# Kernel tuning notes

Hardware: AMD Instinct MI355X
Metric: run time of the kernel (lower is better)

Reference implementation:

```python
import jax, jax.numpy as jnp
import numpy as np

B_, L, DM = 2, 1024, 1024
DIN = 2048            # expand * d_model
HD = 64               # headdim
NH = DIN // HD        # 32 heads
DS = 64               # d_state
NG = 1                # ngroups
TH = NH * (DS // 2)   # theta dim = 1024
SPLITS = np.cumsum([DIN, DIN, NG * DS, NG * DS, NH, TH]).tolist()
EPS = 1e-5

def _rms(x, w):
    return x * jax.lax.rsqrt(jnp.mean(x * x, -1, keepdims=True) + EPS) * w

def setup_inputs():
    ks = jax.random.split(jax.random.key(0), 8)
    d_in = 2 * DIN + 2 * NG * DS + NH + TH + NH  # 5312
    u = jax.random.normal(ks[0], (B_, L, DM), jnp.float32)
    in_proj_w = jax.random.normal(ks[1], (d_in, DM), jnp.float32) * 0.02
    out_proj_w = jax.random.normal(ks[2], (DM, DIN), jnp.float32) * 0.02
    # dt_bias init as in module: inv-softplus of dt ~ logUniform(dt_min, dt_max)
    dt = jnp.exp(jax.random.uniform(ks[3], (NH,)) * (np.log(0.1) - np.log(0.001)) + np.log(0.001))
    dt_bias = dt + jnp.log(-jnp.expm1(-dt))
    A_log = jnp.log(jax.random.uniform(ks[4], (NH,), minval=1.0, maxval=16.0))
    D = jnp.ones((NH,), jnp.float32)
    B_norm_w = jnp.ones((DS,), jnp.float32)
    C_norm_w = jnp.ones((DS,), jnp.float32)
    B_bias = jnp.ones((NH, DS), jnp.float32)
    C_bias = jnp.ones((NH, DS), jnp.float32)
    norm_w = jnp.ones((DIN,), jnp.float32)
    return dict(u=u, in_proj_w=in_proj_w, dt_bias=dt_bias, A_log=A_log, D=D,
                B_norm_w=B_norm_w, C_norm_w=C_norm_w, B_bias=B_bias, C_bias=C_bias,
                norm_w=norm_w, out_proj_w=out_proj_w)

def reference(u, in_proj_w, dt_bias, A_log, D, B_norm_w, C_norm_w, B_bias, C_bias, norm_w, out_proj_w):
    zxbcdt = u @ in_proj_w.T                                  # (b,l,5312)
    z, x, Br, Cr, dtr, thr, lamr = jnp.split(zxbcdt, SPLITS, axis=-1)
    dt = jax.nn.softplus(dtr + dt_bias)                       # (b,l,h)
    A = -jnp.exp(A_log)                                       # (h,) negative
    x = x.reshape(B_, L, NH, HD)
    # BC norm at group level, then group->head expansion, then head-specific bias
    Bg = _rms(Br.reshape(B_, L, NG, DS), B_norm_w)
    Cg = _rms(Cr.reshape(B_, L, NG, DS), C_norm_w)
    Bh = jnp.broadcast_to(Bg, (B_, L, NH, DS)) + B_bias
    Ch = jnp.broadcast_to(Cg, (B_, L, NH, DS)) + C_bias
    # data-dependent RoPE with cumulative angles
    th_cs = jnp.cumsum(thr.reshape(B_, L, NH, DS // 2), axis=1)
    c, s = jnp.cos(th_cs), jnp.sin(th_cs)
    def rot(v):
        v1, v2 = v[..., :DS // 2], v[..., DS // 2:]
        return jnp.concatenate([v1 * c - v2 * s, v1 * s + v2 * c], -1)
    Bh, Ch = rot(Bh), rot(Ch)
    # trapezoidal discretization coefficients
    lam = jax.nn.sigmoid(lamr)                                # (b,l,h) in [0,1]
    alpha = jnp.exp(dt * A)
    gamma = lam * dt
    beta = (1.0 - lam) * dt * alpha
    def step(carry, inp):
        h, bx_prev = carry
        x_t, B_t, C_t, a_t, b_t, g_t = inp
        bx = x_t[..., :, None] * B_t[..., None, :]            # (b,h,p,n)
        h = a_t[..., None, None] * h + b_t[..., None, None] * bx_prev + g_t[..., None, None] * bx
        y = jnp.einsum('bhn,bhpn->bhp', C_t, h)
        return (h, bx), y
    m = lambda t: jnp.moveaxis(t, 1, 0)                       # seq-major for scan
    h0 = jnp.zeros((B_, NH, HD, DS), u.dtype)
    _, ys = jax.lax.scan(step, (h0, h0), (m(x), m(Bh), m(Ch), m(alpha), m(beta), m(gamma)))
    y = jnp.moveaxis(ys, 0, 1) + x * D[:, None]               # D skip, per head
    y = y.reshape(B_, L, DIN)
    # RMSNormGated, norm_before_gate=False: norm(y * silu(z)) * w
    g = y * jax.nn.silu(z)
    out = _rms(g, norm_w)
    return out @ out_proj_w.T
```

## Files before the change

### kernel.cpp

```cpp
#include <hip/hip_runtime.h>
#include <hip/hip_bf16.h>

#define DMODEL 1024
#define DIN    2048
#define NH     32
#define HD     64
#define DS     64
#define LSEQ   1024
#define BB     2
#define DTOT   5312
#define ROWS   (BB*LSEQ)
#define OFF_Z   0
#define OFF_X   2048
#define OFF_BR  4096
#define OFF_CR  4160
#define OFF_DT  4224
#define OFF_TH  4256
#define OFF_LAM 5280
#define NZX     4096
#define NREM    (DTOT - NZX)
#define NSEG 8
#define SEG  (LSEQ / NSEG)

typedef short  s16x8 __attribute__((ext_vector_type(8)));
typedef float  f32x4 __attribute__((ext_vector_type(4)));
typedef unsigned short u16;

__device__ __forceinline__ unsigned int f2bf(float f) {
    unsigned int u = __float_as_uint(f);
    u += 0x7fffu + ((u >> 16) & 1u);
    return u >> 16;
}
__device__ __forceinline__ unsigned int pk(float x, float y) {
    return f2bf(x) | (f2bf(y) << 16);
}
__device__ __forceinline__ void split1(float v, u16& hi, u16& lo) {
    const unsigned int h = f2bf(v);
    hi = (u16)h;
    lo = (u16)f2bf(v - __uint_as_float(h << 16));
}

typedef const __attribute__((address_space(1))) unsigned int glb_u32;
typedef __attribute__((address_space(3))) unsigned int lds_u32;
__device__ __forceinline__ void gload16(const void* g, void* l) {
    __builtin_amdgcn_global_load_lds((glb_u32*)g, (lds_u32*)l, 16, 0, 0);
}

__global__ __launch_bounds__(256) void conv_u(const float* __restrict__ src,
        u16* __restrict__ hi, u16* __restrict__ lo) {
    const size_t i4 = ((size_t)blockIdx.x * 256 + threadIdx.x) * 4;
    const float4 v = *(const float4*)(src + i4);
    const unsigned int h0 = f2bf(v.x), h1 = f2bf(v.y), h2 = f2bf(v.z), h3 = f2bf(v.w);
    uint2 hw, lw;
    hw.x = h0 | (h1 << 16); hw.y = h2 | (h3 << 16);
    lw.x = pk(v.x - __uint_as_float(h0 << 16), v.y - __uint_as_float(h1 << 16));
    lw.y = pk(v.z - __uint_as_float(h2 << 16), v.w - __uint_as_float(h3 << 16));
    *(uint2*)(hi + i4) = hw;
    *(uint2*)(lo + i4) = lw;
}

__global__ __launch_bounds__(256) void conv_w(const float* __restrict__ src,
        u16* __restrict__ hi, u16* __restrict__ lo) {
    const size_t i4 = ((size_t)blockIdx.x * 256 + threadIdx.x) * 4;
    const float4 v = *(const float4*)(src + i4);
    const unsigned int h0 = f2bf(v.x), h1 = f2bf(v.y), h2 = f2bf(v.z), h3 = f2bf(v.w);
    uint2 hw, lw;
    hw.x = h0 | (h1 << 16); hw.y = h2 | (h3 << 16);
    lw.x = pk(v.x - __uint_as_float(h0 << 16), v.y - __uint_as_float(h1 << 16));
    lw.y = pk(v.z - __uint_as_float(h2 << 16), v.w - __uint_as_float(h3 << 16));
    *(uint2*)(hi + i4) = hw;
    if ((i4 >> 10) >= NZX)
        *(uint2*)(lo + (i4 - (size_t)NZX * DMODEL)) = lw;
}

__global__ __launch_bounds__(256) void conv_wo(const float* __restrict__ src,
        u16* __restrict__ hi) {
    const size_t i4 = ((size_t)blockIdx.x * 256 + threadIdx.x) * 4;
    const float4 v = *(const float4*)(src + i4);
    uint2 hw;
    hw.x = pk(v.x, v.y); hw.y = pk(v.z, v.w);
    *(uint2*)(hi + i4) = hw;
}

__global__ __launch_bounds__(256) void mfma_gemm_zx(const u16* __restrict__ uA_,
                                                    const u16* __restrict__ uW,
                                                    float* __restrict__ zx) {
    __shared__ u16 Al[2][128 * 32];
    __shared__ u16 Bl[2][128 * 32];
    const int tid = threadIdx.x;
    const int m0 = blockIdx.y * 128, n0 = blockIdx.x * 128;
    const int lane = tid & 63, wave = tid >> 6;
    const int wr = wave >> 1, wc = wave & 1;
    const int lr = lane >> 4, lc = lane & 15;
    const int sr = tid >> 2;
    const int sc = (tid & 3) * 8;

    f32x4 acc[4][4] = {};

    const u16* pA = uA_ + (size_t)(m0 + sr) * DMODEL + sc;
    const u16* pB = uW  + (size_t)(n0 + sr) * DMODEL + sc;

#define STAGE_ZX(buf, k0) {                                              \
        gload16(pA + (k0), &Al[buf][tid * 8]);                           \
        gload16(pA + (k0) + (size_t)64 * DMODEL, &Al[buf][tid * 8 + 2048]); \
        gload16(pB + (k0), &Bl[buf][tid * 8]);                           \
        gload16(pB + (k0) + (size_t)64 * DMODEL, &Bl[buf][tid * 8 + 2048]); }

    STAGE_ZX(0, 0);
    __syncthreads();
    int cur = 0;
    for (int k0 = 0; k0 < DMODEL; k0 += 32) {
        if (k0 + 32 < DMODEL) STAGE_ZX(cur ^ 1, k0 + 32);
        s16x8 af[4], bf[4];
        #pragma unroll
        for (int f = 0; f < 4; ++f) {
            af[f] = *(const s16x8*)&Al[cur][(wr * 64 + f * 16 + lc) * 32 + lr * 8];
            bf[f] = *(const s16x8*)&Bl[cur][(wc * 64 + f * 16 + lc) * 32 + lr * 8];
        }
        #pragma unroll
        for (int fm = 0; fm < 4; ++fm)
            #pragma unroll
            for (int fn = 0; fn < 4; ++fn)
                acc[fm][fn] = __builtin_amdgcn_mfma_f32_16x16x32_bf16(
                    af[fm], bf[fn], acc[fm][fn], 0, 0, 0);
        __syncthreads();
        cur ^= 1;
    }
#undef STAGE_ZX

    #pragma unroll
    for (int fm = 0; fm < 4; ++fm)
        #pragma unroll
        for (int fn = 0; fn < 4; ++fn) {
            const size_t col = n0 + wc * 64 + fn * 16 + lc;
            #pragma unroll
            for (int j = 0; j < 4; ++j) {
                const size_t row = m0 + wr * 64 + fm * 16 + lr * 4 + j;
                zx[row * DTOT + col] = acc[fm][fn][j];
            }
        }
}

__global__ __launch_bounds__(256) void mfma_gemm_out(const u16* __restrict__ A,
                                                     const u16* __restrict__ B,
                                                     float* __restrict__ C,
                                                     int K, int ldc) {
    __shared__ u16 Als[2][128 * 32];
    __shared__ u16 Bls[2][64 * 32];
    const int tid = threadIdx.x;
    const int m0 = blockIdx.y * 128, n0 = blockIdx.x * 64;
    const int lane = tid & 63, wave = tid >> 6;
    const int wr = wave >> 1, wc = wave & 1;
    const int lr = lane >> 4, lc = lane & 15;
    const int sr = tid >> 2;
    const int sc = (tid & 3) * 8;

    f32x4 acc[4][2] = {};

    const u16* pA = A + (size_t)(m0 + sr) * K + sc;
    const u16* pB = B + (size_t)(n0 + sr) * K + sc;

#define STAGE_OUT(buf, k0) {                                             \
        gload16(pA + (k0), &Als[buf][tid * 8]);                          \
        gload16(pA + (k0) + (size_t)64 * K, &Als[buf][tid * 8 + 2048]);  \
        gload16(pB + (k0), &Bls[buf][tid * 8]); }

    STAGE_OUT(0, 0);
    __syncthreads();
    int cur = 0;
    for (int k0 = 0; k0 < K; k0 += 32) {
        if (k0 + 32 < K) STAGE_OUT(cur ^ 1, k0 + 32);
        s16x8 af[4], bf[2];
        #pragma unroll
        for (int f = 0; f < 4; ++f)
            af[f] = *(const s16x8*)&Als[cur][(wr * 64 + f * 16 + lc) * 32 + lr * 8];
        #pragma unroll
        for (int f = 0; f < 2; ++f)
            bf[f] = *(const s16x8*)&Bls[cur][(wc * 32 + f * 16 + lc) * 32 + lr * 8];
        #pragma unroll
        for (int fm = 0; fm < 4; ++fm)
            #pragma unroll
            for (int fn = 0; fn < 2; ++fn)
                acc[fm][fn] = __builtin_amdgcn_mfma_f32_16x16x32_bf16(
                    af[fm], bf[fn], acc[fm][fn], 0, 0, 0);
        __syncthreads();
        cur ^= 1;
    }
#undef STAGE_OUT

    #pragma unroll
    for (int fm = 0; fm < 4; ++fm)
        #pragma unroll
        for (int fn = 0; fn < 2; ++fn) {
            const size_t col = n0 + wc * 32 + fn * 16 + lc;
            #pragma unroll
            for (int j = 0; j < 4; ++j) {
                const size_t row = m0 + wr * 64 + fm * 16 + lr * 4 + j;
                C[row * (size_t)ldc + col] = acc[fm][fn][j];
            }
        }
}

__global__ __launch_bounds__(256) void mfma_gemm_rem3(const u16* __restrict__ uh,
        const u16* __restrict__ ul, const u16* __restrict__ wh,
        const u16* __restrict__ wl, float* __restrict__ zxr) {
    __shared__ u16 Ah[2][128 * 32], Alo[2][128 * 32];
    __shared__ u16 Bh[2][64 * 32],  Blo[2][64 * 32];
    const int tid = threadIdx.x;
    const int m0 = blockIdx.y * 128, n0 = blockIdx.x * 64;
    const int lane = tid & 63, wave = tid >> 6;
    const int wr = wave >> 1, wc = wave & 1;
    const int lr = lane >> 4, lc = lane & 15;
    const int sr = tid >> 2;
    const int sc = (tid & 3) * 8;

    f32x4 acc[4][2] = {};

    const u16* pAh = uh + (size_t)(m0 + sr) * DMODEL + sc;
    const u16* pAl = ul + (size_t)(m0 + sr) * DMODEL + sc;
    const u16* pBh = wh + (size_t)(n0 + sr) * DMODEL + sc;
    const u16* pBl = wl + (size_t)(n0 + sr) * DMODEL + sc;

#define STAGE_R3(buf, k0) {                                                  \
        gload16(pAh + (k0), &Ah[buf][tid * 8]);                              \
        gload16(pAh + (k0) + (size_t)64 * DMODEL, &Ah[buf][tid * 8 + 2048]); \
        gload16(pAl + (k0), &Alo[buf][tid * 8]);                             \
        gload16(pAl + (k0) + (size_t)64 * DMODEL, &Alo[buf][tid * 8 + 2048]);\
        gload16(pBh + (k0), &Bh[buf][tid * 8]);                              \
        gload16(pBl + (k0), &Blo[buf][tid * 8]); }

    STAGE_R3(0, 0);
    __syncthreads();
    int cur = 0;
    for (int k0 = 0; k0 < DMODEL; k0 += 32) {
        if (k0 + 32 < DMODEL) STAGE_R3(cur ^ 1, k0 + 32);
        s16x8 ahf[4], alf[4], bhf[2], blf[2];
        #pragma unroll
        for (int f = 0; f < 4; ++f) {
            ahf[f] = *(const s16x8*)&Ah[cur][(wr * 64 + f * 16 + lc) * 32 + lr * 8];
            alf[f] = *(const s16x8*)&Alo[cur][(wr * 64 + f * 16 + lc) * 32 + lr * 8];
        }
        #pragma unroll
        for (int f = 0; f < 2; ++f) {
            bhf[f] = *(const s16x8*)&Bh[cur][(wc * 32 + f * 16 + lc) * 32 + lr * 8];
            blf[f] = *(const s16x8*)&Blo[cur][(wc * 32 + f * 16 + lc) * 32 + lr * 8];
        }
        #pragma unroll
        for (int fm = 0; fm < 4; ++fm)
            #pragma unroll
            for (int fn = 0; fn < 2; ++fn) {
                acc[fm][fn] = __builtin_amdgcn_mfma_f32_16x16x32_bf16(
                    ahf[fm], bhf[fn], acc[fm][fn], 0, 0, 0);
                acc[fm][fn] = __builtin_amdgcn_mfma_f32_16x16x32_bf16(
                    ahf[fm], blf[fn], acc[fm][fn], 0, 0, 0);
                acc[fm][fn] = __builtin_amdgcn_mfma_f32_16x16x32_bf16(
                    alf[fm], bhf[fn], acc[fm][fn], 0, 0, 0);
            }
        __syncthreads();
        cur ^= 1;
    }
#undef STAGE_R3

    #pragma unroll
    for (int fm = 0; fm < 4; ++fm)
        #pragma unroll
        for (int fn = 0; fn < 2; ++fn) {
            const size_t col = n0 + wc * 32 + fn * 16 + lc;
            #pragma unroll
            for (int j = 0; j < 4; ++j) {
                const size_t row = m0 + wr * 64 + fm * 16 + lr * 4 + j;
                zxr[row * DTOT + col] = acc[fm][fn][j];
            }
        }
}

__global__ __launch_bounds__(64) void prep_kernel(const float* __restrict__ zx,
        const float* __restrict__ dt_bias, const float* __restrict__ A_log,
        const float* __restrict__ B_norm_w, const float* __restrict__ C_norm_w,
        float* __restrict__ Bg, float* __restrict__ Cg,
        float4* __restrict__ abg4) {
    const int bl = blockIdx.x;
    const int b = bl >> 10, l = bl & (LSEQ - 1);
    const int t  = threadIdx.x;
    const float* row = zx + (size_t)bl * DTOT;
    const float br = row[OFF_BR + t];
    const float cr = row[OFF_CR + t];
    float ssb = br * br, ssc = cr * cr;
    #pragma unroll
    for (int k = 1; k < 64; k <<= 1) { ssb += __shfl_xor(ssb, k); ssc += __shfl_xor(ssc, k); }
    const float scB = rsqrtf(ssb * (1.f / 64.f) + 1e-5f);
    const float scC = rsqrtf(ssc * (1.f / 64.f) + 1e-5f);
    Bg[(size_t)bl * 64 + t] = br * scB * B_norm_w[t];
    Cg[(size_t)bl * 64 + t] = cr * scC * C_norm_w[t];
    if (t < NH) {
        const float dtr = row[OFF_DT + t] + dt_bias[t];
        const float dt  = (dtr > 20.f) ? dtr : log1pf(expf(dtr));
        const float lamr = row[OFF_LAM + t];
        const float lam  = 1.f / (1.f + expf(-lamr));
        const float Ah   = -expf(A_log[t]);
        const float al   = expf(dt * Ah);
        const float bp   = (1.f - lam) * dt;
        const size_t o = ((size_t)b * NH + t) * LSEQ + l;
        abg4[o] = make_float4(al, bp * al, lam * dt, bp);
    }
}

__global__ __launch_bounds__(256) void cumsum_kernel(const float* __restrict__ zx,
                                                     float* __restrict__ th_cs) {
    const int bh = blockIdx.x;
    const int b = bh >> 5, h = bh & 31;
    const int d = threadIdx.x & 31, seg = threadIdx.x >> 5;
    const float* base = zx + (size_t)b * LSEQ * DTOT + OFF_TH + h * 32 + d;
    float* out = th_cs + (size_t)b * LSEQ * 1024 + h * 32 + d;
    __shared__ float sums[8][33];
    const int l0 = seg * 128;
    float s = 0.f;
    #pragma unroll 4
    for (int i = 0; i < 128; ++i) s += base[(size_t)(l0 + i) * DTOT];
    sums[seg][d] = s;
    __syncthreads();
    float acc = 0.f;
    for (int s2 = 0; s2 < seg; ++s2) acc += sums[s2][d];
    #pragma unroll 4
    for (int i = 0; i < 128; ++i) {
        acc += base[(size_t)(l0 + i) * DTOT];
        out[(size_t)(l0 + i) * 1024] = acc;
    }
}

__global__ __launch_bounds__(256) void rot_kernel(const float* __restrict__ th_cs,
        const float* __restrict__ Bg, const float* __restrict__ Cg,
        const float* __restrict__ B_bias, const float* __restrict__ C_bias,
        float* __restrict__ Brot, float* __restrict__ Crot) {
    const size_t idx = (size_t)blockIdx.x * 256 + threadIdx.x;
    const int j = (int)(idx & 31);
    const int h = (int)((idx >> 5) & 31);
    const size_t bl = idx >> 10;
    const int l = (int)(bl & (LSEQ - 1));
    const int b = (int)(bl >> 10);
    const float th = th_cs[idx];
    float s, c;
    sincosf(th, &s, &c);
    float v1 = Bg[bl * 64 + j]      + B_bias[h * 64 + j];
    float v2 = Bg[bl * 64 + 32 + j] + B_bias[h * 64 + 32 + j];
    const size_t ob = ((size_t)(b * NH + h) * LSEQ + l) * DS + j;
    Brot[ob]      = v1 * c - v2 * s;
    Brot[ob + 32] = v1 * s + v2 * c;
    v1 = Cg[bl * 64 + j]      + C_bias[h * 64 + j];
    v2 = Cg[bl * 64 + 32 + j] + C_bias[h * 64 + 32 + j];
    Crot[ob]      = v1 * c - v2 * s;
    Crot[ob + 32] = v1 * s + v2 * c;
}

__global__ __launch_bounds__(64) void wcalc_kernel(const float4* __restrict__ abg4,
        float* __restrict__ wbuf, float* __restrict__ aprod,
        float* __restrict__ bscale, float* __restrict__ Lbuf) {
    const int bh = blockIdx.x;
    const int lane = threadIdx.x;
    const int seg = lane >> 3, sub = lane & 7;
    const int t0 = seg * SEG;
    const int sbase = t0 + sub * 16;
    const float4* ab = abg4 + (size_t)bh * LSEQ;

    float part = 0.f;
    #pragma unroll
    for (int i = 0; i < 16; ++i) part += logf(ab[sbase + i].x);
    float incl = part;
    #pragma unroll
    for (int d = 1; d < 8; d <<= 1) {
        const float v = __shfl_up(incl, d, 8);
        if (sub >= d) incl += v;
    }
    const float LE = __shfl(incl, 7, 8);
    float Lrun = incl - part;

    for (int i = 0; i < 16; ++i) {
        const int s = sbase + i;
        const float4 A = ab[s];
        Lrun += logf(A.x);
        Lbuf[(size_t)bh * LSEQ + s] = Lrun;
        float w;
        if ((s & (SEG - 1)) == (SEG - 1)) w = A.z;
        else w = __expf(LE - Lrun) * (A.z + ab[s + 1].w);
        wbuf[(size_t)bh * LSEQ + s] = w;
    }
    if (sub == 0) {
        aprod[bh * NSEG + seg] = __expf(LE);
        bscale[bh * NSEG + seg] = (seg > 0) ? __expf(LE) * ab[t0].w : 0.f;
    }
}

#define WK 136
__global__ __launch_bounds__(256) void hseg_gemm(const float* __restrict__ zx,
        const float* __restrict__ Brot, const float* __restrict__ wbuf,
        float* __restrict__ hseg) {
    __shared__ u16 XH[64][WK], XL[64][WK], BHs[64][WK], BLs[64][WK];
    const int blk = blockIdx.x;
    const int seg = blk & (NSEG - 1), bh = blk >> 3;
    const int b = bh >> 5, h = bh & 31;
    const int tid = threadIdx.x;

    {
        const int sIdx = tid >> 1, half = tid & 1;
        const int t = seg * SEG + sIdx;
        const float wv = wbuf[(size_t)bh * LSEQ + t];
        const float* xsrc = zx + ((size_t)b * LSEQ + t) * DTOT + OFF_X + h * 64 + half * 32;
        const float* bsrc = Brot + ((size_t)bh * LSEQ + t) * DS + half * 32;
        #pragma unroll
        for (int i = 0; i < 32; i += 4) {
            const float4 xv = *(const float4*)(xsrc + i);
            const float4 bv = *(const float4*)(bsrc + i);
            const int p0 = half * 32 + i;
            u16 hi, lo;
            split1(xv.x * wv, hi, lo); XH[p0 + 0][sIdx] = hi; XL[p0 + 0][sIdx] = lo;
            split1(xv.y * wv, hi, lo); XH[p0 + 1][sIdx] = hi; XL[p0 + 1][sIdx] = lo;
            split1(xv.z * wv, hi, lo); XH[p0 + 2][sIdx] = hi; XL[p0 + 2][sIdx] = lo;
            split1(xv.w * wv, hi, lo); XH[p0 + 3][sIdx] = hi; XL[p0 + 3][sIdx] = lo;
            split1(bv.x, hi, lo); BHs[p0 + 0][sIdx] = hi; BLs[p0 + 0][sIdx] = lo;
            split1(bv.y, hi, lo); BHs[p0 + 1][sIdx] = hi; BLs[p0 + 1][sIdx] = lo;
            split1(bv.z, hi, lo); BHs[p0 + 2][sIdx] = hi; BLs[p0 + 2][sIdx] = lo;
            split1(bv.w, hi, lo); BHs[p0 + 3][sIdx] = hi; BLs[p0 + 3][sIdx] = lo;
        }
    }
    __syncthreads();

    const int lane = tid & 63, wave = tid >> 6;
    const int wR = wave >> 1, wC = wave & 1;
    const int lr = lane >> 4, lc = lane & 15;

    f32x4 acc[2][2] = {};
    #pragma unroll
    for (int ks = 0; ks < 4; ++ks) {
        const int k0 = ks * 32;
        s16x8 xh[2], xl[2], bhf[2], blf[2];
        #pragma unroll
        for (int f = 0; f < 2; ++f) {
            const int pr = wR * 32 + f * 16 + lc;
            xh[f] = *(const s16x8*)&XH[pr][k0 + lr * 8];
            xl[f] = *(const s16x8*)&XL[pr][k0 + lr * 8];
            const int nr = wC * 32 + f * 16 + lc;
            bhf[f] = *(const s16x8*)&BHs[nr][k0 + lr * 8];
            blf[f] = *(const s16x8*)&BLs[nr][k0 + lr * 8];
        }
        #pragma unroll
        for (int fm = 0; fm < 2; ++fm)
            #pragma unroll
            for (int fn = 0; fn < 2; ++fn) {
                acc[fm][fn] = __builtin_amdgcn_mfma_f32_16x16x32_bf16(
                    xh[fm], bhf[fn], acc[fm][fn], 0, 0, 0);
                acc[fm][fn] = __builtin_amdgcn_mfma_f32_16x16x32_bf16(
                    xh[fm], blf[fn], acc[fm][fn], 0, 0, 0);
                acc[fm][fn] = __builtin_amdgcn_mfma_f32_16x16x32_bf16(
                    xl[fm], bhf[fn], acc[fm][fn], 0, 0, 0);
            }
    }

    float* hp = hseg + ((size_t)(bh * NSEG + seg) * HD) * DS;
    #pragma unroll
    for (int fm = 0; fm < 2; ++fm)
        #pragma unroll
        for (int fn = 0; fn < 2; ++fn) {
            const int n = wC * 32 + fn * 16 + lc;
            #pragma unroll
            for (int j = 0; j < 4; ++j) {
                const int p = wR * 32 + fm * 16 + lr * 4 + j;
                hp[p * DS + n] = acc[fm][fn][j];
            }
        }
}

__global__ __launch_bounds__(256) void scan_fix(float* __restrict__ hseg,
        const float* __restrict__ aprod, const float* __restrict__ bscale,
        const float* __restrict__ zx, const float* __restrict__ Brot,
        const float4* __restrict__ abg4) {
    const int blk = blockIdx.x;
    const int ptile = blk & 3, h = (blk >> 2) & 31, b = blk >> 7;
    const int tid = threadIdx.x;
    const int pl = tid >> 4, ng = tid & 15;
    const int p = ptile * 16 + pl;
    const int n0 = ng * 4;
    const size_t bh = (size_t)b * NH + h;

    float4 cur = make_float4(0.f, 0.f, 0.f, 0.f);
    #pragma unroll
    for (int s = 0; s < NSEG; ++s) {
        float* hp = hseg + (((bh * NSEG + s) * HD + p) * DS + n0);
        float4 tmp = *(const float4*)hp;
        float4 hst = cur;
        if (s > 0) {
            const float bs = bscale[bh * NSEG + s];
            const float bp0 = abg4[bh * LSEQ + s * SEG].w;
            const int tm1 = s * SEG - 1;
            const float4 Bm = *(const float4*)(Brot + ((size_t)bh * LSEQ + tm1) * DS + n0);
            const float xm = zx[((size_t)b * LSEQ + tm1) * DTOT + OFF_X + h * HD + p];
            const float fb = bs * xm;
            const float f1 = bp0 * xm;
            tmp.x = fmaf(fb, Bm.x, tmp.x);
            tmp.y = fmaf(fb, Bm.y, tmp.y);
            tmp.z = fmaf(fb, Bm.z, tmp.z);
            tmp.w = fmaf(fb, Bm.w, tmp.w);
            hst.x = fmaf(f1, Bm.x, hst.x);
            hst.y = fmaf(f1, Bm.y, hst.y);
            hst.z = fmaf(f1, Bm.z, hst.z);
            hst.w = fmaf(f1, Bm.w, hst.w);
        }
        *(float4*)hp = hst;
        const float a = aprod[bh * NSEG + s];
        cur.x = fmaf(a, cur.x, tmp.x);
        cur.y = fmaf(a, cur.y, tmp.y);
        cur.z = fmaf(a, cur.z, tmp.z);
        cur.w = fmaf(a, cur.w, tmp.w);
    }
}

#define GK   72
#define GWK2 136
__global__ __launch_bounds__(256) void ssd_y(const float* __restrict__ zx,
        const float* __restrict__ Brot, const float* __restrict__ Crot,
        const float4* __restrict__ abg4, const float* __restrict__ hseg,
        const float* __restrict__ Lbuf, const float* __restrict__ Dp,
        float* __restrict__ yb) {
    __shared__ u16 sm[50176];
    __shared__ float Ls[128], gbs[128], gms[128], eLs[128];
    u16* CH = sm;
    u16* CL = sm + 9216;
    u16* BHl = sm + 18432;
    u16* BLl = sm + 27648;
    u16* GH = sm;
    u16* GL = sm + 17408;
    u16* XTH = sm + 36864;
    u16* HH  = sm + 45568;

    const int blk = blockIdx.x;
    const int seg = blk & (NSEG - 1), bh = blk >> 3;
    const int b = bh >> 5, h = bh & 31;
    const int tid = threadIdx.x;
    const int t0 = seg * SEG;
    const int lane = tid & 63, wave = tid >> 6;
    const int wr = wave >> 1, wc = wave & 1;
    const int lr = lane >> 4, lc = lane & 15;

    {
        const int r = tid >> 1, half = tid & 1;
        const float* csrc = Crot + ((size_t)bh * LSEQ + t0 + r) * DS + half * 32;
        const float* bsrc = Brot + ((size_t)bh * LSEQ + t0 + r) * DS + half * 32;
        const float* xsrc = zx + ((size_t)b * LSEQ + t0 + r) * DTOT + OFF_X + h * 64 + half * 32;
        #pragma unroll
        for (int i = 0; i < 32; i += 4) {
            const float4 cv = *(const float4*)(csrc + i);
            const float4 bv = *(const float4*)(bsrc + i);
            const float4 xv = *(const float4*)(xsrc + i);
            const int c0 = half * 32 + i;
            u16 hi, lo;
            split1(cv.x, hi, lo); CH[r * GK + c0 + 0] = hi; CL[r * GK + c0 + 0] = lo;
            split1(cv.y, hi, lo); CH[r * GK + c0 + 1] = hi; CL[r * GK + c0 + 1] = lo;
            split1(cv.z, hi, lo); CH[r * GK + c0 + 2] = hi; CL[r * GK + c0 + 2] = lo;
            split1(cv.w, hi, lo); CH[r * GK + c0 + 3] = hi; CL[r * GK + c0 + 3] = lo;
            split1(bv.x, hi, lo); BHl[r * GK + c0 + 0] = hi; BLl[r * GK + c0 + 0] = lo;
            split1(bv.y, hi, lo); BHl[r * GK + c0 + 1] = hi; BLl[r * GK + c0 + 1] = lo;
            split1(bv.z, hi, lo); BHl[r * GK + c0 + 2] = hi; BLl[r * GK + c0 + 2] = lo;
            split1(bv.w, hi, lo); BHl[r * GK + c0 + 3] = hi; BLl[r * GK + c0 + 3] = lo;
            XTH[(c0 + 0) * GWK2 + r] = (u16)f2bf(xv.x);
            XTH[(c0 + 1) * GWK2 + r] = (u16)f2bf(xv.y);
            XTH[(c0 + 2) * GWK2 + r] = (u16)f2bf(xv.z);
            XTH[(c0 + 3) * GWK2 + r] = (u16)f2bf(xv.w);
        }
    }
    {
        const int p = tid >> 2, q = (tid & 3) * 16;
        const float* hsrc = hseg + (((size_t)(bh * NSEG + seg)) * HD + p) * DS + q;
        #pragma unroll
        for (int i = 0; i < 16; i += 4) {
            const float4 hv = *(const float4*)(hsrc + i);
            HH[p * GK + q + i + 0] = (u16)f2bf(hv.x);
            HH[p * GK + q + i + 1] = (u16)f2bf(hv.y);
            HH[p * GK + q + i + 2] = (u16)f2bf(hv.z);
            HH[p * GK + q + i + 3] = (u16)f2bf(hv.w);
        }
    }
    if (tid < 128) {
        const int t = t0 + tid;
        const float4 A = abg4[(size_t)bh * LSEQ + t];
        const float Lv = Lbuf[(size_t)bh * LSEQ + t];
        Ls[tid] = Lv;
        gms[tid] = A.z;
        gbs[tid] = (tid < 127) ? A.z + abg4[(size_t)bh * LSEQ + t + 1].w : 0.f;
        eLs[tid] = __expf(Lv);
    }
    __syncthreads();

    f32x4 accP[4][2] = {};
    #pragma unroll
    for (int ks = 0; ks < 2; ++ks) {
        const int k0 = ks * 32;
        s16x8 ch[4], cl4[4], hh2[2];
        #pragma unroll
        for (int f = 0; f < 4; ++f) {
            const int row = wr * 64 + f * 16 + lc;
            ch[f]  = *(const s16x8*)&CH[row * GK + k0 + lr * 8];
            cl4[f] = *(const s16x8*)&CL[row * GK + k0 + lr * 8];
        }
        #pragma unroll
        for (int f = 0; f < 2; ++f) {
            const int row = wc * 32 + f * 16 + lc;
            hh2[f] = *(const s16x8*)&HH[row * GK + k0 + lr * 8];
        }
        #pragma unroll
        for (int fm = 0; fm < 4; ++fm)
            #pragma unroll
            for (int fn = 0; fn < 2; ++fn) {
                accP[fm][fn] = __builtin_amdgcn_mfma_f32_16x16x32_bf16(
                    ch[fm], hh2[fn], accP[fm][fn], 0, 0, 0);
                accP[fm][fn] = __builtin_amdgcn_mfma_f32_16x16x32_bf16(
                    cl4[fm], hh2[fn], accP[fm][fn], 0, 0, 0);
            }
    }
    f32x4 accY[4][2];
    #pragma unroll
    for (int fm = 0; fm < 4; ++fm)
        #pragma unroll
        for (int fn = 0; fn < 2; ++fn)
            #pragma unroll
            for (int jj = 0; jj < 4; ++jj) {
                const int i = wr * 64 + fm * 16 + lr * 4 + jj;
                accY[fm][fn][jj] = eLs[i] * accP[fm][fn][jj];
            }

    f32x4 accG[4][4] = {};
    #pragma unroll
    for (int ks = 0; ks < 2; ++ks) {
        const int k0 = ks * 32;
        s16x8 ch[4], cl4[4], bh4[4], bl4[4];
        #pragma unroll
        for (int f = 0; f < 4; ++f) {
            const int rowc = wr * 64 + f * 16 + lc;
            ch[f]  = *(const s16x8*)&CH[rowc * GK + k0 + lr * 8];
            cl4[f] = *(const s16x8*)&CL[rowc * GK + k0 + lr * 8];
            const int rowb = wc * 64 + f * 16 + lc;
            bh4[f] = *(const s16x8*)&BHl[rowb * GK + k0 + lr * 8];
            bl4[f] = *(const s16x8*)&BLl[rowb * GK + k0 + lr * 8];
        }
        #pragma unroll
        for (int fm = 0; fm < 4; ++fm)
            #pragma unroll
            for (int fn = 0; fn < 4; ++fn) {
                accG[fm][fn] = __builtin_amdgcn_mfma_f32_16x16x32_bf16(
                    ch[fm], bh4[fn], accG[fm][fn], 0, 0, 0);
                accG[fm][fn] = __builtin_amdgcn_mfma_f32_16x16x32_bf16(
                    ch[fm], bl4[fn], accG[fm][fn], 0, 0, 0);
                accG[fm][fn] = __builtin_amdgcn_mfma_f32_16x16x32_bf16(
                    cl4[fm], bh4[fn], accG[fm][fn], 0, 0, 0);
            }
    }
    __syncthreads();

    #pragma unroll
    for (int fm = 0; fm < 4; ++fm)
        #pragma unroll
        for (int fn = 0; fn < 4; ++fn)
            #pragma unroll
            for (int jj = 0; jj < 4; ++jj) {
                const int i = wr * 64 + fm * 16 + lr * 4 + jj;
                const int j = wc * 64 + fn * 16 + lc;
                float w;
                if (j < i)      w = __expf(Ls[i] - Ls[j]) * gbs[j];
                else if (j == i) w = gms[i];
                else             w = 0.f;
                const float v = accG[fm][fn][jj] * w;
                u16 hi, lo; split1(v, hi, lo);
                GH[i * GWK2 + j] = hi;
                GL[i * GWK2 + j] = lo;
            }
    __syncthreads();

    #pragma unroll
    for (int ks = 0; ks < 4; ++ks) {
        const int k0 = ks * 32;
        s16x8 gh4[4], gl4[4], xf[2];
        #pragma unroll
        for (int f = 0; f < 4; ++f) {
            const int row = wr * 64 + f * 16 + lc;
            gh4[f] = *(const s16x8*)&GH[row * GWK2 + k0 + lr * 8];
            gl4[f] = *(const s16x8*)&GL[row * GWK2 + k0 + lr * 8];
        }
        #pragma unroll
        for (int f = 0; f < 2; ++f) {
            const int row = wc * 32 + f * 16 + lc;
            xf[f] = *(const s16x8*)&XTH[row * GWK2 + k0 + lr * 8];
        }
        #pragma unroll
        for (int fm = 0; fm < 4; ++fm)
            #pragma unroll
            for (int fn = 0; fn < 2; ++fn) {
                accY[fm][fn] = __builtin_amdgcn_mfma_f32_16x16x32_bf16(
                    gh4[fm], xf[fn], accY[fm][fn], 0, 0, 0);
                accY[fm][fn] = __builtin_amdgcn_mfma_f32_16x16x32_bf16(
                    gl4[fm], xf[fn], accY[fm][fn], 0, 0, 0);
            }
    }

    const float Dh = Dp[h];
    #pragma unroll
    for (int fm = 0; fm < 4; ++fm)
        #pragma unroll
        for (int fn = 0; fn < 2; ++fn) {
            const int p = wc * 32 + fn * 16 + lc;
            #pragma unroll
            for (int jj = 0; jj < 4; ++jj) {
                const int i = wr * 64 + fm * 16 + lr * 4 + jj;
                const float xv = __uint_as_float(((unsigned)XTH[p * GWK2 + i]) << 16);
                yb[((size_t)b * LSEQ + t0 + i) * DIN + h * 64 + p] =
                    accY[fm][fn][jj] + Dh * xv;
            }
        }
}

__global__ __launch_bounds__(256) void gate_norm_kernel(const float* __restrict__ yb,
        const float* __restrict__ zx, const float* __restrict__ norm_w,
        u16* __restrict__ gnb) {
    const int bl = blockIdx.x;
    const int tid = threadIdx.x;
    const float* yrow = yb + (size_t)bl * DIN;
    const float* zrow = zx + (size_t)bl * DTOT + OFF_Z;
    float g[8];
    float ss = 0.f;
    #pragma unroll
    for (int i = 0; i < 8; ++i) {
        const int c = tid + i * 256;
        const float yv = yrow[c];
        const float zv = zrow[c];
        const float sg = 1.f / (1.f + expf(-zv));
        const float gv = yv * zv * sg;
        g[i] = gv;
        ss += gv * gv;
    }
    #pragma unroll
    for (int k = 1; k < 64; k <<= 1) ss += __shfl_xor(ss, k);
    __shared__ float wsum[4];
    if ((tid & 63) == 0) wsum[tid >> 6] = ss;
    __syncthreads();
    ss = wsum[0] + wsum[1] + wsum[2] + wsum[3];
    const float sc = rsqrtf(ss * (1.f / 2048.f) + 1e-5f);
    #pragma unroll
    for (int i = 0; i < 8; ++i) {
        const int c = tid + i * 256;
        gnb[(size_t)bl * DIN + c] = (u16)f2bf(g[i] * sc * norm_w[c]);
    }
}

extern "C" void kernel_launch(void* const* d_in, const int* in_sizes, int n_in,
                              void* d_out, int out_size, void* d_ws, size_t ws_size,
                              hipStream_t stream) {
    const float* u          = (const float*)d_in[0];
    const float* in_proj_w  = (const float*)d_in[1];
    const float* dt_bias    = (const float*)d_in[2];
    const float* A_log      = (const float*)d_in[3];
    const float* Dp         = (const float*)d_in[4];
    const float* B_norm_w   = (const float*)d_in[5];
    const float* C_norm_w   = (const float*)d_in[6];
    const float* B_bias     = (const float*)d_in[7];
    const float* C_bias     = (const float*)d_in[8];
    const float* norm_w     = (const float*)d_in[9];
    const float* out_proj_w = (const float*)d_in[10];
    float* out = (float*)d_out;

    float* p = (float*)d_ws;
    float* zx    = p; p += (size_t)ROWS * DTOT;
    float* th_cs = p; p += (size_t)ROWS * 1024;
    float* Brot  = p; p += (size_t)ROWS * 2048;
    float* Crot  = p; p += (size_t)ROWS * 2048;
    float* Bg    = p; p += (size_t)ROWS * 64;
    float* Cg    = p; p += (size_t)ROWS * 64;
    float4* abg4 = (float4*)p; p += (size_t)ROWS * NH * 4;
    float* yb    = p; p += (size_t)ROWS * 2048;
    float* hseg   = th_cs;
    float* aprod  = Bg;
    float* bscale = Bg + 512;
    float* Lbuf   = Bg + 2048;
    float* wbuf   = Cg;

    u16* u_bf = (u16*)Brot;
    u16* u_lo = u_bf + (size_t)ROWS * DMODEL;
    u16* w_bf = u_lo + (size_t)ROWS * DMODEL;
    u16* w_lo = w_bf + (size_t)DTOT * DMODEL;
    u16* gn_bf = (u16*)Brot;
    u16* wo_bf = gn_bf + (size_t)ROWS * DIN;

    conv_u<<<(ROWS * DMODEL / 4) / 256, 256, 0, stream>>>(u, u_bf, u_lo);
    conv_w<<<((size_t)DTOT * DMODEL / 4) / 256, 256, 0, stream>>>(in_proj_w, w_bf, w_lo);
    mfma_gemm_zx<<<dim3(NZX / 128, ROWS / 128), 256, 0, stream>>>(u_bf, w_bf, zx);
    mfma_gemm_rem3<<<dim3(NREM / 64, ROWS / 128), 256, 0, stream>>>(
        u_bf, u_lo, w_bf + (size_t)NZX * DMODEL, w_lo, zx + NZX);
    prep_kernel<<<ROWS, 64, 0, stream>>>(zx, dt_bias, A_log, B_norm_w, C_norm_w,
                                         Bg, Cg, abg4);
    cumsum_kernel<<<BB * NH, 256, 0, stream>>>(zx, th_cs);
    rot_kernel<<<(ROWS * 1024) / 256, 256, 0, stream>>>(th_cs, Bg, Cg, B_bias, C_bias,
                                                        Brot, Crot);
    wcalc_kernel<<<BB * NH, 64, 0, stream>>>(abg4, wbuf, aprod, bscale, Lbuf);
    hseg_gemm<<<BB * NH * NSEG, 256, 0, stream>>>(zx, Brot, wbuf, hseg);
    scan_fix<<<BB * NH * 4, 256, 0, stream>>>(hseg, aprod, bscale, zx, Brot, abg4);
    ssd_y<<<BB * NH * NSEG, 256, 0, stream>>>(zx, Brot, Crot, abg4, hseg, Lbuf, Dp, yb);
    conv_wo<<<(DMODEL * DIN / 4) / 256, 256, 0, stream>>>(out_proj_w, wo_bf);
    gate_norm_kernel<<<ROWS, 256, 0, stream>>>(yb, zx, norm_w, gn_bf);
    mfma_gemm_out<<<dim3(DMODEL / 64, ROWS / 128), 256, 0, stream>>>(
        gn_bf, wo_bf, out, DIN, DMODEL);
}
```

Before: 209.4 us.

## Load SSD operands directly from global into MFMA fragments, skipping LDS staging

The ssd_y kernel no longer stages C, B, X and the segment state through LDS as split bf16 hi/lo arrays. Each wave now reads its fragments straight from global memory and splits them in registers. The C·H and C·B products are merged into one k-loop, and the weighted G matrix is kept in LDS as fp32 and split when loaded. This removes the staging pass and a barrier and shrinks LDS use so that two blocks can fit per CU (launch_bounds 256,2). The cost is redundant, poorly coalesced global loads, especially the strided scalar X reads down the DTOT stride, and duplicated split arithmetic.

```diff
diff --git a/kernel.cpp b/kernel.cpp
--- a/kernel.cpp
+++ b/kernel.cpp
@@ -38,6 +38,24 @@
     const unsigned int h = f2bf(v);
     hi = (u16)h;
     lo = (u16)f2bf(v - __uint_as_float(h << 16));
+}
+__device__ __forceinline__ void split8(const float4 a, const float4 b,
+                                       s16x8& hi, s16x8& lo) {
+    u16 h_, l_;
+    split1(a.x, h_, l_); hi[0] = (short)h_; lo[0] = (short)l_;
+    split1(a.y, h_, l_); hi[1] = (short)h_; lo[1] = (short)l_;
+    split1(a.z, h_, l_); hi[2] = (short)h_; lo[2] = (short)l_;
+    split1(a.w, h_, l_); hi[3] = (short)h_; lo[3] = (short)l_;
+    split1(b.x, h_, l_); hi[4] = (short)h_; lo[4] = (short)l_;
+    split1(b.y, h_, l_); hi[5] = (short)h_; lo[5] = (short)l_;
+    split1(b.z, h_, l_); hi[6] = (short)h_; lo[6] = (short)l_;
+    split1(b.w, h_, l_); hi[7] = (short)h_; lo[7] = (short)l_;
+}
+__device__ __forceinline__ void cvt8(const float4 a, const float4 b, s16x8& hi) {
+    hi[0] = (short)f2bf(a.x); hi[1] = (short)f2bf(a.y);
+    hi[2] = (short)f2bf(a.z); hi[3] = (short)f2bf(a.w);
+    hi[4] = (short)f2bf(b.x); hi[5] = (short)f2bf(b.y);
+    hi[6] = (short)f2bf(b.z); hi[7] = (short)f2bf(b.w);
 }
 
 typedef const __attribute__((address_space(1))) unsigned int glb_u32;
@@ -513,23 +531,14 @@
     }
 }
 
-#define GK   72
-#define GWK2 136
-__global__ __launch_bounds__(256) void ssd_y(const float* __restrict__ zx,
+#define GWF 132
+__global__ __launch_bounds__(256, 2) void ssd_y(const float* __restrict__ zx,
         const float* __restrict__ Brot, const float* __restrict__ Crot,
         const float4* __restrict__ abg4, const float* __restrict__ hseg,
         const float* __restrict__ Lbuf, const float* __restrict__ Dp,
         float* __restrict__ yb) {
-    __shared__ u16 sm[50176];
+    __shared__ float Gw[128 * GWF];
     __shared__ float Ls[128], gbs[128], gms[128], eLs[128];
-    u16* CH = sm;
-    u16* CL = sm + 9216;
-    u16* BHl = sm + 18432;
-    u16* BLl = sm + 27648;
-    u16* GH = sm;
-    u16* GL = sm + 17408;
-    u16* XTH = sm + 36864;
-    u16* HH  = sm + 45568;
 
     const int blk = blockIdx.x;
     const int seg = blk & (NSEG - 1), bh = blk >> 3;
@@ -540,44 +549,6 @@
     const int wr = wave >> 1, wc = wave & 1;
     const int lr = lane >> 4, lc = lane & 15;
 
-    {
-        const int r = tid >> 1, half = tid & 1;
-        const float* csrc = Crot + ((size_t)bh * LSEQ + t0 + r) * DS + half * 32;
-        const float* bsrc = Brot + ((size_t)bh * LSEQ + t0 + r) * DS + half * 32;
-        const float* xsrc = zx + ((size_t)b * LSEQ + t0 + r) * DTOT + OFF_X + h * 64 + half * 32;
-        #pragma unroll
-        for (int i = 0; i < 32; i += 4) {
-            const float4 cv = *(const float4*)(csrc + i);
-            const float4 bv = *(const float4*)(bsrc + i);
-            const float4 xv = *(const float4*)(xsrc + i);
-            const int c0 = half * 32 + i;
-            u16 hi, lo;
-            split1(cv.x, hi, lo); CH[r * GK + c0 + 0] = hi; CL[r * GK + c0 + 0] = lo;
-            split1(cv.y, hi, lo); CH[r * GK + c0 + 1] = hi; CL[r * GK + c0 + 1] = lo;
-            split1(cv.z, hi, lo); CH[r * GK + c0 + 2] = hi; CL[r * GK + c0 + 2] = lo;
-            split1(cv.w, hi, lo); CH[r * GK + c0 + 3] = hi; CL[r * GK + c0 + 3] = lo;
-            split1(bv.x, hi, lo); BHl[r * GK + c0 + 0] = hi; BLl[r * GK + c0 + 0] = lo;
-            split1(bv.y, hi, lo); BHl[r * GK + c0 + 1] = hi; BLl[r * GK + c0 + 1] = lo;
-            split1(bv.z, hi, lo); BHl[r * GK + c0 + 2] = hi; BLl[r * GK + c0 + 2] = lo;
-            split1(bv.w, hi, lo); BHl[r * GK + c0 + 3] = hi; BLl[r * GK + c0 + 3] = lo;
-            XTH[(c0 + 0) * GWK2 + r] = (u16)f2bf(xv.x);
-            XTH[(c0 + 1) * GWK2 + r] = (u16)f2bf(xv.y);
-            XTH[(c0 + 2) * GWK2 + r] = (u16)f2bf(xv.z);
-            XTH[(c0 + 3) * GWK2 + r] = (u16)f2bf(xv.w);
-        }
-    }
-    {
-        const int p = tid >> 2, q = (tid & 3) * 16;
-        const float* hsrc = hseg + (((size_t)(bh * NSEG + seg)) * HD + p) * DS + q;
-        #pragma unroll
-        for (int i = 0; i < 16; i += 4) {
-            const float4 hv = *(const float4*)(hsrc + i);
-            HH[p * GK + q + i + 0] = (u16)f2bf(hv.x);
-            HH[p * GK + q + i + 1] = (u16)f2bf(hv.y);
-            HH[p * GK + q + i + 2] = (u16)f2bf(hv.z);
-            HH[p * GK + q + i + 3] = (u16)f2bf(hv.w);
-        }
-    }
     if (tid < 128) {
         const int t = t0 + tid;
         const float4 A = abg4[(size_t)bh * LSEQ + t];
@@ -589,59 +560,36 @@
     }
     __syncthreads();
 
+    const float* Cbase = Crot + ((size_t)bh * LSEQ + t0) * DS;
+    const float* Bbase = Brot + ((size_t)bh * LSEQ + t0) * DS;
+    const float* Hbase = hseg + ((size_t)(bh * NSEG + seg) * HD) * DS;
+
     f32x4 accP[4][2] = {};
+    f32x4 accG[4][4] = {};
     #pragma unroll
     for (int ks = 0; ks < 2; ++ks) {
-        const int k0 = ks * 32;
-        s16x8 ch[4], cl4[4], hh2[2];
-        #pragma unroll
-        for (int f = 0; f < 4; ++f) {
-            const int row = wr * 64 + f * 16 + lc;
-            ch[f]  = *(const s16x8*)&CH[row * GK + k0 + lr * 8];
-            cl4[f] = *(const s16x8*)&CL[row * GK + k0 + lr * 8];
-        }
-        #pragma unroll
-        for (int f = 0; f < 2; ++f) {
-            const int row = wc * 32 + f * 16 + lc;
-            hh2[f] = *(const s16x8*)&HH[row * GK + k0 + lr * 8];
-        }
-        #pragma unroll
-        for (int fm = 0; fm < 4; ++fm)
-            #pragma unroll
-            for (int fn = 0; fn < 2; ++fn) {
-                accP[fm][fn] = __builtin_amdgcn_mfma_f32_16x16x32_bf16(
-                    ch[fm], hh2[fn], accP[fm][fn], 0, 0, 0);
-                accP[fm][fn] = __builtin_amdgcn_mfma_f32_16x16x32_bf16(
-                    cl4[fm], hh2[fn], accP[fm][fn], 0, 0, 0);
-            }
-    }
-    f32x4 accY[4][2];
-    #pragma unroll
-    for (int fm = 0; fm < 4; ++fm)
-        #pragma unroll
-        for (int fn = 0; fn < 2; ++fn)
-            #pragma unroll
-            for (int jj = 0; jj < 4; ++jj) {
-                const int i = wr * 64 + fm * 16 + lr * 4 + jj;
-                accY[fm][fn][jj] = eLs[i] * accP[fm][fn][jj];
-            }
-
-    f32x4 accG[4][4] = {};
-    #pragma unroll
-    for (int ks = 0; ks < 2; ++ks) {
-        const int k0 = ks * 32;
-        s16x8 ch[4], cl4[4], bh4[4], bl4[4];
+        const int k0 = ks * 32 + lr * 8;
+        s16x8 ch[4], cl4[4], bh4[4], bl4[4], hh2[2];
         #pragma unroll
         for (int f = 0; f < 4; ++f) {
             const int rowc = wr * 64 + f * 16 + lc;
-            ch[f]  = *(const s16x8*)&CH[rowc * GK + k0 + lr * 8];
-            cl4[f] = *(const s16x8*)&CL[rowc * GK + k0 + lr * 8];
+            const float4 c0 = *(const float4*)(Cbase + (size_t)rowc * DS + k0);
+            const float4 c1 = *(const float4*)(Cbase + (size_t)rowc * DS + k0 + 4);
+            split8(c0, c1, ch[f], cl4[f]);
             const int rowb = wc * 64 + f * 16 + lc;
-            bh4[f] = *(const s16x8*)&BHl[rowb * GK + k0 + lr * 8];
-            bl4[f] = *(const s16x8*)&BLl[rowb * GK + k0 + lr * 8];
-        }
-        #pragma unroll
-        for (int fm = 0; fm < 4; ++fm)
+            const float4 b0 = *(const float4*)(Bbase + (size_t)rowb * DS + k0);
+            const float4 b1 = *(const float4*)(Bbase + (size_t)rowb * DS + k0 + 4);
+            split8(b0, b1, bh4[f], bl4[f]);
+        }
+        #pragma unroll
+        for (int f = 0; f < 2; ++f) {
+            const int rowp = wc * 32 + f * 16 + lc;
+            const float4 h0 = *(const float4*)(Hbase + (size_t)rowp * DS + k0);
+            const float4 h1 = *(const float4*)(Hbase + (size_t)rowp * DS + k0 + 4);
+            cvt8(h0, h1, hh2[f]);
+        }
+        #pragma unroll
+        for (int fm = 0; fm < 4; ++fm) {
             #pragma unroll
             for (int fn = 0; fn < 4; ++fn) {
                 accG[fm][fn] = __builtin_amdgcn_mfma_f32_16x16x32_bf16(
@@ -651,8 +599,15 @@
                 accG[fm][fn] = __builtin_amdgcn_mfma_f32_16x16x32_bf16(
                     cl4[fm], bh4[fn], accG[fm][fn], 0, 0, 0);
             }
-    }
-    __syncthreads();
+            #pragma unroll
+            for (int fn = 0; fn < 2; ++fn) {
+                accP[fm][fn] = __builtin_amdgcn_mfma_f32_16x16x32_bf16(
+                    ch[fm], hh2[fn], accP[fm][fn], 0, 0, 0);
+                accP[fm][fn] = __builtin_amdgcn_mfma_f32_16x16x32_bf16(
+                    cl4[fm], hh2[fn], accP[fm][fn], 0, 0, 0);
+            }
+        }
+    }
 
     #pragma unroll
     for (int fm = 0; fm < 4; ++fm)
@@ -663,30 +618,42 @@
                 const int i = wr * 64 + fm * 16 + lr * 4 + jj;
                 const int j = wc * 64 + fn * 16 + lc;
                 float w;
-                if (j < i)      w = __expf(Ls[i] - Ls[j]) * gbs[j];
+                if (j < i)       w = __expf(Ls[i] - Ls[j]) * gbs[j];
                 else if (j == i) w = gms[i];
                 else             w = 0.f;
-                const float v = accG[fm][fn][jj] * w;
-                u16 hi, lo; split1(v, hi, lo);
-                GH[i * GWK2 + j] = hi;
-                GL[i * GWK2 + j] = lo;
+                Gw[i * GWF + j] = accG[fm][fn][jj] * w;
+            }
+
+    f32x4 accY[4][2];
+    #pragma unroll
+    for (int fm = 0; fm < 4; ++fm)
+        #pragma unroll
+        for (int fn = 0; fn < 2; ++fn)
+            #pragma unroll
+            for (int jj = 0; jj < 4; ++jj) {
+                const int i = wr * 64 + fm * 16 + lr * 4 + jj;
+                accY[fm][fn][jj] = eLs[i] * accP[fm][fn][jj];
             }
     __syncthreads();
 
+    const float* Xbase = zx + ((size_t)b * LSEQ + t0) * DTOT + OFF_X + h * 64;
     #pragma unroll
     for (int ks = 0; ks < 4; ++ks) {
-        const int k0 = ks * 32;
+        const int k0 = ks * 32 + lr * 8;
         s16x8 gh4[4], gl4[4], xf[2];
         #pragma unroll
         for (int f = 0; f < 4; ++f) {
-            const int row = wr * 64 + f * 16 + lc;
-            gh4[f] = *(const s16x8*)&GH[row * GWK2 + k0 + lr * 8];
-            gl4[f] = *(const s16x8*)&GL[row * GWK2 + k0 + lr * 8];
+            const int rowi = wr * 64 + f * 16 + lc;
+            const float4 g0 = *(const float4*)&Gw[rowi * GWF + k0];
+            const float4 g1 = *(const float4*)&Gw[rowi * GWF + k0 + 4];
+            split8(g0, g1, gh4[f], gl4[f]);
         }
         #pragma unroll
         for (int f = 0; f < 2; ++f) {
-            const int row = wc * 32 + f * 16 + lc;
-            xf[f] = *(const s16x8*)&XTH[row * GWK2 + k0 + lr * 8];
+            const int rowp = wc * 32 + f * 16 + lc;
+            #pragma unroll
+            for (int q = 0; q < 8; ++q)
+                xf[f][q] = (short)f2bf(Xbase[(size_t)(k0 + q) * DTOT + rowp]);
         }
         #pragma unroll
         for (int fm = 0; fm < 4; ++fm)
@@ -708,7 +675,8 @@
             #pragma unroll
             for (int jj = 0; jj < 4; ++jj) {
                 const int i = wr * 64 + fm * 16 + lr * 4 + jj;
-                const float xv = __uint_as_float(((unsigned)XTH[p * GWK2 + i]) << 16);
+                const float xv = __uint_as_float(
+                    f2bf(Xbase[(size_t)i * DTOT + p]) << 16);
                 yb[((size_t)b * LSEQ + t0 + i) * DIN + h * 64 + p] =
                     accY[fm][fn][jj] + Dh * xv;
             }
```

New measurement: 199.0 us. 1.05x faster.
